# Kernel tuning notes

Hardware: AMD Instinct MI355X
Metric: run time of the kernel (lower is better)

Reference implementation:

```python
import jax, jax.numpy as jnp
import numpy as np

B, N_IN, HID, N_OUT = 1024, 512, 64, 256


def setup_inputs() -> dict:
    key = jax.random.key(0)
    ks = jax.random.split(key, 10)
    s = 0.02
    return {
        "x": jax.random.normal(ks[0], (B, N_IN), dtype=jnp.float32),
        "ln_gamma": jnp.ones((N_IN,), dtype=jnp.float32),
        "ln_beta": jnp.zeros((N_IN,), dtype=jnp.float32),
        "Wq": jax.random.normal(ks[1], (N_IN, HID * N_OUT), dtype=jnp.float32) * s,
        "bq": jnp.zeros((HID * N_OUT,), dtype=jnp.float32),
        "Wk": jax.random.normal(ks[2], (N_IN, HID * N_OUT), dtype=jnp.float32) * s,
        "bk": jnp.zeros((HID * N_OUT,), dtype=jnp.float32),
        "Wv": jax.random.normal(ks[3], (N_IN, HID * N_OUT), dtype=jnp.float32) * s,
        "bv": jnp.zeros((HID * N_OUT,), dtype=jnp.float32),
        "Wo": jax.random.normal(ks[4], (HID, N_OUT), dtype=jnp.float32) * s,
        "bo": jnp.zeros((N_OUT,), dtype=jnp.float32),
    }


def reference(x, ln_gamma, ln_beta, Wq, bq, Wk, bk, Wv, bv, Wo, bo):
    # LayerNorm over last dim (input_shape)
    mu = jnp.mean(x, axis=-1, keepdims=True)
    var = jnp.mean(jnp.square(x - mu), axis=-1, keepdims=True)
    h = (x - mu) / jnp.sqrt(var + 1e-5) * ln_gamma + ln_beta  # (B, 512)

    # QKV projections, then view as (B, N_OUT, HID)
    q = (h @ Wq + bq).reshape(B, N_OUT, HID)
    k = (h @ Wk + bk).reshape(B, N_OUT, HID)
    v = (h @ Wv + bv).reshape(B, N_OUT, HID)

    # Single-head scaled dot-product attention over length N_OUT
    w = jnp.einsum("bqc,bkc->bqk", q, k) * (HID ** -0.5)
    w = jax.nn.softmax(w, axis=2)
    a = jnp.einsum("bqk,bkc->bqc", w, v)  # (B, N_OUT, HID)

    # Output projection, ReLU, negate -> seminegative contact map
    out = jax.nn.relu(a @ Wo + bo)  # (B, N_OUT, N_OUT)
    return -out
```

## Files before the change

kernel.cpp:

```cpp
#include <hip/hip_runtime.h>
#include <hip/hip_fp16.h>

typedef _Float16 h4_t __attribute__((ext_vector_type(4)));
typedef _Float16 h8_t __attribute__((ext_vector_type(8)));
typedef float f4_t __attribute__((ext_vector_type(4)));

#define B_SZ 1024
#define N_IN 512
#define HID 64
#define N_OUT 256
#define QKN (N_OUT * HID)

__global__ __launch_bounds__(256) void k_ln(const float* __restrict__ x,
                                            const float* __restrict__ gamma,
                                            const float* __restrict__ beta,
                                            _Float16* __restrict__ h16) {
    int tid = threadIdx.x;
    int wave = tid >> 6, lane = tid & 63;
    int row = blockIdx.x * 4 + wave;
    const float4* xr = (const float4*)(x + (size_t)row * N_IN);
    float4 a = xr[lane];
    float4 b = xr[lane + 64];
    float s = a.x + a.y + a.z + a.w + b.x + b.y + b.z + b.w;
    float sq = a.x * a.x + a.y * a.y + a.z * a.z + a.w * a.w +
               b.x * b.x + b.y * b.y + b.z * b.z + b.w * b.w;
    for (int off = 1; off < 64; off <<= 1) {
        s += __shfl_xor(s, off);
        sq += __shfl_xor(sq, off);
    }
    float mean = s * (1.0f / N_IN);
    float var = sq * (1.0f / N_IN) - mean * mean;
    float rstd = rsqrtf(var + 1e-5f);
    float4 g0 = ((const float4*)gamma)[lane];
    float4 g1 = ((const float4*)gamma)[lane + 64];
    float4 e0 = ((const float4*)beta)[lane];
    float4 e1 = ((const float4*)beta)[lane + 64];
    h4_t o0 = {(_Float16)((a.x - mean) * rstd * g0.x + e0.x),
               (_Float16)((a.y - mean) * rstd * g0.y + e0.y),
               (_Float16)((a.z - mean) * rstd * g0.z + e0.z),
               (_Float16)((a.w - mean) * rstd * g0.w + e0.w)};
    h4_t o1 = {(_Float16)((b.x - mean) * rstd * g1.x + e1.x),
               (_Float16)((b.y - mean) * rstd * g1.y + e1.y),
               (_Float16)((b.z - mean) * rstd * g1.z + e1.z),
               (_Float16)((b.w - mean) * rstd * g1.w + e1.w)};
    h4_t* hr = (h4_t*)(h16 + (size_t)row * N_IN);
    hr[lane] = o0;
    hr[lane + 64] = o1;
}

__global__ __launch_bounds__(256) void k_wt(const float* __restrict__ Wq,
                                            const float* __restrict__ Wk,
                                            const float* __restrict__ Wv,
                                            _Float16* __restrict__ wt) {
    __shared__ _Float16 t[64][65];
    const float* W = blockIdx.z == 0 ? Wq : (blockIdx.z == 1 ? Wk : Wv);
    _Float16* out = wt + (size_t)blockIdx.z * ((size_t)QKN * N_IN);
    int n0 = blockIdx.x * 64, k0 = blockIdx.y * 64;
    int c = threadIdx.x & 63, rq = threadIdx.x >> 6;
    for (int i = 0; i < 16; i++) {
        int r = i * 4 + rq;
        t[r][c] = (_Float16)W[(size_t)(k0 + r) * QKN + n0 + c];
    }
    __syncthreads();
    for (int i = 0; i < 16; i++) {
        int r = i * 4 + rq;
        out[(size_t)(n0 + r) * N_IN + k0 + c] = t[c][r];
    }
}

__global__ __launch_bounds__(256) void k_qkv(const _Float16* __restrict__ h16,
                                             const _Float16* __restrict__ wt,
                                             const float* __restrict__ bq,
                                             const float* __restrict__ bk,
                                             const float* __restrict__ bv,
                                             _Float16* __restrict__ qkv) {
    __shared__ _Float16 As[2][4096];
    __shared__ _Float16 Bs[2][4096];
    int z = blockIdx.z;
    const _Float16* Wb = wt + (size_t)z * ((size_t)QKN * N_IN);
    const float* bias = z == 0 ? bq : (z == 1 ? bk : bv);
    _Float16* out = qkv + (size_t)z * ((size_t)B_SZ * QKN);
    int m0 = blockIdx.x * 128, n0 = blockIdx.y * 128;
    int tid = threadIdx.x, lane = tid & 63, w = tid >> 6;
    int wm = w & 1, wn = w >> 1;
    int col16 = lane & 15, quad = lane >> 4;

    int idx0 = (w * 2 + 0) * 512 + lane * 8;
    int idx1 = (w * 2 + 1) * 512 + lane * 8;
    int row0 = idx0 >> 5, col0 = idx0 & 31;
    int row1 = idx1 >> 5, col1 = idx1 & 31;
    const _Float16* pa0 = h16 + (size_t)(m0 + row0) * N_IN + col0;
    const _Float16* pa1 = h16 + (size_t)(m0 + row1) * N_IN + col1;
    const _Float16* pb0 = Wb + (size_t)(n0 + row0) * N_IN + col0;
    const _Float16* pb1 = Wb + (size_t)(n0 + row1) * N_IN + col1;

#define STAGE_QKV(buf, kk)                                                          \
    do {                                                                            \
        __builtin_amdgcn_global_load_lds(                                           \
            (const __attribute__((address_space(1))) void*)(pa0 + (kk)),            \
            (__attribute__((address_space(3))) void*)(&As[buf][(w * 2 + 0) * 512]), \
            16, 0, 0);                                                              \
        __builtin_amdgcn_global_load_lds(                                           \
            (const __attribute__((address_space(1))) void*)(pa1 + (kk)),            \
            (__attribute__((address_space(3))) void*)(&As[buf][(w * 2 + 1) * 512]), \
            16, 0, 0);                                                              \
        __builtin_amdgcn_global_load_lds(                                           \
            (const __attribute__((address_space(1))) void*)(pb0 + (kk)),            \
            (__attribute__((address_space(3))) void*)(&Bs[buf][(w * 2 + 0) * 512]), \
            16, 0, 0);                                                              \
        __builtin_amdgcn_global_load_lds(                                           \
            (const __attribute__((address_space(1))) void*)(pb1 + (kk)),            \
            (__attribute__((address_space(3))) void*)(&Bs[buf][(w * 2 + 1) * 512]), \
            16, 0, 0);                                                              \
    } while (0)

#define QKV_COMPUTE(buf)                                                                        \
    do {                                                                                        \
        h8_t af[4], bf[4];                                                                      \
        for (int mt = 0; mt < 4; mt++)                                                          \
            af[mt] = *(const h8_t*)(&As[buf][(wm * 64 + mt * 16 + col16) * 32 + quad * 8]);     \
        for (int nt = 0; nt < 4; nt++)                                                          \
            bf[nt] = *(const h8_t*)(&Bs[buf][(wn * 64 + nt * 16 + col16) * 32 + quad * 8]);     \
        for (int mt = 0; mt < 4; mt++)                                                          \
            for (int nt = 0; nt < 4; nt++)                                                      \
                acc[mt][nt] =                                                                   \
                    __builtin_amdgcn_mfma_f32_16x16x32_f16(bf[nt], af[mt], acc[mt][nt], 0, 0, 0); \
    } while (0)

    f4_t acc[4][4] = {};
    STAGE_QKV(0, 0);
    STAGE_QKV(1, 32);
    for (int t = 0; t < 14; t++) {
        int buf = t & 1;
        asm volatile("s_waitcnt vmcnt(4)" ::: "memory");
        __builtin_amdgcn_s_barrier();
        asm volatile("" ::: "memory");
        QKV_COMPUTE(buf);
        asm volatile("s_waitcnt lgkmcnt(0)" ::: "memory");
        __builtin_amdgcn_s_barrier();
        asm volatile("" ::: "memory");
        STAGE_QKV(buf, (t + 2) * 32);
    }
    asm volatile("s_waitcnt vmcnt(4)" ::: "memory");
    __builtin_amdgcn_s_barrier();
    asm volatile("" ::: "memory");
    QKV_COMPUTE(0);
    asm volatile("s_waitcnt vmcnt(0)" ::: "memory");
    __builtin_amdgcn_s_barrier();
    asm volatile("" ::: "memory");
    QKV_COMPUTE(1);
#undef STAGE_QKV
#undef QKV_COMPUTE

    for (int mt = 0; mt < 4; mt++) {
        int m = m0 + wm * 64 + mt * 16 + col16;
        for (int nt = 0; nt < 4; nt++) {
            int nb = n0 + wn * 64 + nt * 16 + quad * 4;
            f4_t bb = *(const f4_t*)(bias + nb);
            h4_t hv = {(_Float16)(acc[mt][nt][0] + bb[0]),
                       (_Float16)(acc[mt][nt][1] + bb[1]),
                       (_Float16)(acc[mt][nt][2] + bb[2]),
                       (_Float16)(acc[mt][nt][3] + bb[3])};
            *(h4_t*)(out + (size_t)m * QKN + nb) = hv;
        }
    }
}

__global__ __launch_bounds__(512) void k_attn(const _Float16* __restrict__ qkv,
                                              const float* __restrict__ Wo,
                                              const float* __restrict__ bo,
                                              float* __restrict__ out) {
    __shared__ _Float16 lds[32768];
    int b = blockIdx.x;
    int tid = threadIdx.x, lane = tid & 63, w = tid >> 6;
    int col16 = lane & 15, quad = lane >> 4;
    const _Float16* qb = qkv + (size_t)b * QKN;
    const _Float16* kb = qkv + (size_t)(B_SZ + b) * QKN;
    const _Float16* vb = qkv + (size_t)(2 * B_SZ + b) * QKN;

    for (int r = 0; r < 4; r++) {
        int slab = r * 8 + w;
        int c8 = slab >> 2, kblk = slab & 3;
        __builtin_amdgcn_global_load_lds(
            (const __attribute__((address_space(1))) void*)(kb + (size_t)(kblk * 64 + lane) * 64 + c8 * 8),
            (__attribute__((address_space(3))) void*)(lds + slab * 512),
            16, 0, 0);
    }

    int kq_ = lane >> 2, k3 = lane & 3;
    int hb = w & 3, kbase2 = (w >> 2) * 128;
    for (int kc2 = 0; kc2 < 2; kc2++) {
        int key = kbase2 + kc2 * 64 + lane;
        h8_t va = *(const h8_t*)(vb + (size_t)key * 64 + hb * 16);
        h8_t vc = *(const h8_t*)(vb + (size_t)key * 64 + hb * 16 + 8);
        int kq = key >> 2;
        int kx = kq & 7;
        _Float16* vp = lds + 16384 + kq * 256 + k3;
        for (int j = 0; j < 8; j++) vp[(size_t)((hb * 16 + j) ^ kx) * 4] = va[j];
        for (int j = 0; j < 8; j++) vp[(size_t)((hb * 16 + 8 + j) ^ kx) * 4] = vc[j];
    }
    (void)kq_;

    h8_t qf[2][2];
    int qbase = w * 32;
    for (int qt = 0; qt < 2; qt++)
        for (int ki = 0; ki < 2; ki++)
            qf[qt][ki] = *(const h8_t*)(qb + (size_t)(qbase + qt * 16 + col16) * 64 + ki * 32 + quad * 8);

    __syncthreads();

    f4_t o[4][2] = {};
    float lrun[2] = {0.f, 0.f};
    const float sc = 0.125f * 1.44269504f;

    for (int kc = 0; kc < 16; kc++) {
        h8_t kf0 = *(const h8_t*)(lds + (size_t)quad * 2048 + (size_t)(kc * 16 + col16) * 8);
        h8_t kf1 = *(const h8_t*)(lds + (size_t)(4 + quad) * 2048 + (size_t)(kc * 16 + col16) * 8);
        int kqr = kc * 4 + quad, kxr = kqr & 7;
        h4_t vf[4];
        for (int mt = 0; mt < 4; mt++)
            vf[mt] = *(const h4_t*)(lds + 16384 + kqr * 256 +
                                    (size_t)((mt * 16 + col16) ^ kxr) * 4);
        for (int qt = 0; qt < 2; qt++) {
            f4_t s = {};
            s = __builtin_amdgcn_mfma_f32_16x16x32_f16(kf0, qf[qt][0], s, 0, 0, 0);
            s = __builtin_amdgcn_mfma_f32_16x16x32_f16(kf1, qf[qt][1], s, 0, 0, 0);
            float p0 = exp2f(s[0] * sc);
            float p1 = exp2f(s[1] * sc);
            float p2 = exp2f(s[2] * sc);
            float p3 = exp2f(s[3] * sc);
            lrun[qt] += (p0 + p1) + (p2 + p3);
            h4_t pf = {(_Float16)p0, (_Float16)p1, (_Float16)p2, (_Float16)p3};
            for (int mt = 0; mt < 4; mt++)
                o[mt][qt] = __builtin_amdgcn_mfma_f32_16x16x16f16(vf[mt], pf, o[mt][qt], 0, 0, 0);
        }
    }

    for (int qt = 0; qt < 2; qt++) {
        float l = lrun[qt];
        l += __shfl_xor(l, 16);
        l += __shfl_xor(l, 32);
        lrun[qt] = l;
    }

    h4_t af[2][4];
    for (int qt = 0; qt < 2; qt++) {
        float rl = 1.0f / lrun[qt];
        for (int hk = 0; hk < 4; hk++) {
            f4_t t = o[hk][qt];
            af[qt][hk] = (h4_t){(_Float16)(t[0] * rl), (_Float16)(t[1] * rl),
                                (_Float16)(t[2] * rl), (_Float16)(t[3] * rl)};
        }
    }
    __syncthreads();
    {
        int no = tid & 255, pr = tid >> 8;
        for (int it2 = 0; it2 < 8; it2++) {
            int hh0 = it2 * 8 + pr * 4;
            h4_t wv = {(_Float16)Wo[(size_t)(hh0 + 0) * 256 + no],
                       (_Float16)Wo[(size_t)(hh0 + 1) * 256 + no],
                       (_Float16)Wo[(size_t)(hh0 + 2) * 256 + no],
                       (_Float16)Wo[(size_t)(hh0 + 3) * 256 + no]};
            *(h4_t*)(lds + (it2 * 2 + pr) * 1024 + no * 4) = wv;
        }
    }
    __syncthreads();

    float* outb = out + (size_t)b * (N_OUT * N_OUT);
    for (int nc = 0; nc < 4; nc++) {
        for (int nt = 0; nt < 4; nt++) {
            int no = nc * 64 + nt * 16 + col16;
            h4_t wf[4];
            for (int hk = 0; hk < 4; hk++)
                wf[hk] = *(const h4_t*)(lds + (hk * 4 + quad) * 1024 + no * 4);
            f4_t bb = *(const f4_t*)(bo + nc * 64 + nt * 16 + quad * 4);
            for (int qt = 0; qt < 2; qt++) {
                f4_t a = {};
                for (int hk = 0; hk < 4; hk++)
                    a = __builtin_amdgcn_mfma_f32_16x16x16f16(wf[hk], af[qt][hk], a, 0, 0, 0);
                int q = qbase + qt * 16 + col16;
                int nob = nc * 64 + nt * 16 + quad * 4;
                f4_t v;
                for (int r = 0; r < 4; r++) {
                    float t = a[r] + bb[r];
                    v[r] = (t > 0.f) ? -t : 0.f;
                }
                *(f4_t*)(outb + (size_t)q * N_OUT + nob) = v;
            }
        }
    }
}

extern "C" void kernel_launch(void* const* d_in, const int* in_sizes, int n_in,
                              void* d_out, int out_size, void* d_ws, size_t ws_size,
                              hipStream_t stream) {
    const float* x = (const float*)d_in[0];
    const float* gamma = (const float*)d_in[1];
    const float* beta = (const float*)d_in[2];
    const float* Wq = (const float*)d_in[3];
    const float* bq = (const float*)d_in[4];
    const float* Wk = (const float*)d_in[5];
    const float* bk = (const float*)d_in[6];
    const float* Wv = (const float*)d_in[7];
    const float* bv = (const float*)d_in[8];
    const float* Wo = (const float*)d_in[9];
    const float* bo = (const float*)d_in[10];
    float* out = (float*)d_out;

    _Float16* h16 = (_Float16*)d_ws;
    _Float16* wt16 = h16 + (size_t)B_SZ * N_IN;
    _Float16* qkv16 = wt16 + (size_t)3 * QKN * N_IN;

    k_ln<<<dim3(B_SZ / 4), 256, 0, stream>>>(x, gamma, beta, h16);
    k_wt<<<dim3(QKN / 64, N_IN / 64, 3), 256, 0, stream>>>(Wq, Wk, Wv, wt16);
    k_qkv<<<dim3(B_SZ / 128, QKN / 128, 3), 256, 0, stream>>>(h16, wt16, bq, bk, bv, qkv16);
    k_attn<<<dim3(B_SZ), 512, 0, stream>>>(qkv16, Wo, bo, out);
}
```

Baseline: 509.9 us.

## Triple-buffer QKV GEMM and split output projection into separate kernel

The QKV GEMM main loop moves from double to triple buffering in LDS, keeping two stages of loads in flight, and the loop is fully unrolled. The attention kernel no longer stages K in LDS. It reads K fragments straight from global memory and halves its LDS use, which may raise occupancy. The output projection becomes its own kernel, k_proj, which writes normalized attention output through an fp16 workspace and uses a swizzled Wo tile in LDS. The cost is an extra round trip through global memory for the attention output and one more kernel launch.

After: 545.5 us. +7.0%, slower.

```diff
diff --git a/kernel.cpp b/kernel.cpp
--- a/kernel.cpp
+++ b/kernel.cpp
@@ -74,8 +74,8 @@
                                              const float* __restrict__ bk,
                                              const float* __restrict__ bv,
                                              _Float16* __restrict__ qkv) {
-    __shared__ _Float16 As[2][4096];
-    __shared__ _Float16 Bs[2][4096];
+    __shared__ _Float16 As[3][4096];
+    __shared__ _Float16 Bs[3][4096];
     int z = blockIdx.z;
     const _Float16* Wb = wt + (size_t)z * ((size_t)QKN * N_IN);
     const float* bias = z == 0 ? bq : (z == 1 ? bk : bv);
@@ -114,41 +114,41 @@
             16, 0, 0);                                                              \
     } while (0)
 
-#define QKV_COMPUTE(buf)                                                                        \
-    do {                                                                                        \
-        h8_t af[4], bf[4];                                                                      \
-        for (int mt = 0; mt < 4; mt++)                                                          \
-            af[mt] = *(const h8_t*)(&As[buf][(wm * 64 + mt * 16 + col16) * 32 + quad * 8]);     \
-        for (int nt = 0; nt < 4; nt++)                                                          \
-            bf[nt] = *(const h8_t*)(&Bs[buf][(wn * 64 + nt * 16 + col16) * 32 + quad * 8]);     \
-        for (int mt = 0; mt < 4; mt++)                                                          \
-            for (int nt = 0; nt < 4; nt++)                                                      \
-                acc[mt][nt] =                                                                   \
+#define QKV_COMPUTE(buf)                                                                          \
+    do {                                                                                          \
+        h8_t af[4], bf[4];                                                                        \
+        for (int mt = 0; mt < 4; mt++)                                                            \
+            af[mt] = *(const h8_t*)(&As[buf][(wm * 64 + mt * 16 + col16) * 32 + quad * 8]);       \
+        for (int nt = 0; nt < 4; nt++)                                                            \
+            bf[nt] = *(const h8_t*)(&Bs[buf][(wn * 64 + nt * 16 + col16) * 32 + quad * 8]);       \
+        for (int mt = 0; mt < 4; mt++)                                                            \
+            for (int nt = 0; nt < 4; nt++)                                                        \
+                acc[mt][nt] =                                                                     \
                     __builtin_amdgcn_mfma_f32_16x16x32_f16(bf[nt], af[mt], acc[mt][nt], 0, 0, 0); \
     } while (0)
 
     f4_t acc[4][4] = {};
     STAGE_QKV(0, 0);
     STAGE_QKV(1, 32);
-    for (int t = 0; t < 14; t++) {
-        int buf = t & 1;
-        asm volatile("s_waitcnt vmcnt(4)" ::: "memory");
+    STAGE_QKV(2, 64);
+#pragma unroll
+    for (int t = 0; t < 16; t++) {
+        int bi = t % 3;
+        if (t <= 13) {
+            asm volatile("s_waitcnt vmcnt(8)" ::: "memory");
+        } else if (t == 14) {
+            asm volatile("s_waitcnt vmcnt(4)" ::: "memory");
+        } else {
+            asm volatile("s_waitcnt vmcnt(0)" ::: "memory");
+        }
         __builtin_amdgcn_s_barrier();
         asm volatile("" ::: "memory");
-        QKV_COMPUTE(buf);
+        QKV_COMPUTE(bi);
         asm volatile("s_waitcnt lgkmcnt(0)" ::: "memory");
         __builtin_amdgcn_s_barrier();
         asm volatile("" ::: "memory");
-        STAGE_QKV(buf, (t + 2) * 32);
-    }
-    asm volatile("s_waitcnt vmcnt(4)" ::: "memory");
-    __builtin_amdgcn_s_barrier();
-    asm volatile("" ::: "memory");
-    QKV_COMPUTE(0);
-    asm volatile("s_waitcnt vmcnt(0)" ::: "memory");
-    __builtin_amdgcn_s_barrier();
-    asm volatile("" ::: "memory");
-    QKV_COMPUTE(1);
+        if (t + 3 <= 15) STAGE_QKV(bi, (t + 3) * 32);
+    }
 #undef STAGE_QKV
 #undef QKV_COMPUTE
 
@@ -167,10 +167,8 @@
 }
 
 __global__ __launch_bounds__(512) void k_attn(const _Float16* __restrict__ qkv,
-                                              const float* __restrict__ Wo,
-                                              const float* __restrict__ bo,
-                                              float* __restrict__ out) {
-    __shared__ _Float16 lds[32768];
+                                              _Float16* __restrict__ a16) {
+    __shared__ _Float16 lds[16384];
     int b = blockIdx.x;
     int tid = threadIdx.x, lane = tid & 63, w = tid >> 6;
     int col16 = lane & 15, quad = lane >> 4;
@@ -178,16 +176,7 @@
     const _Float16* kb = qkv + (size_t)(B_SZ + b) * QKN;
     const _Float16* vb = qkv + (size_t)(2 * B_SZ + b) * QKN;
 
-    for (int r = 0; r < 4; r++) {
-        int slab = r * 8 + w;
-        int c8 = slab >> 2, kblk = slab & 3;
-        __builtin_amdgcn_global_load_lds(
-            (const __attribute__((address_space(1))) void*)(kb + (size_t)(kblk * 64 + lane) * 64 + c8 * 8),
-            (__attribute__((address_space(3))) void*)(lds + slab * 512),
-            16, 0, 0);
-    }
-
-    int kq_ = lane >> 2, k3 = lane & 3;
+    int k3 = lane & 3;
     int hb = w & 3, kbase2 = (w >> 2) * 128;
     for (int kc2 = 0; kc2 < 2; kc2++) {
         int key = kbase2 + kc2 * 64 + lane;
@@ -195,11 +184,10 @@
         h8_t vc = *(const h8_t*)(vb + (size_t)key * 64 + hb * 16 + 8);
         int kq = key >> 2;
         int kx = kq & 7;
-        _Float16* vp = lds + 16384 + kq * 256 + k3;
+        _Float16* vp = lds + kq * 256 + k3;
         for (int j = 0; j < 8; j++) vp[(size_t)((hb * 16 + j) ^ kx) * 4] = va[j];
         for (int j = 0; j < 8; j++) vp[(size_t)((hb * 16 + 8 + j) ^ kx) * 4] = vc[j];
     }
-    (void)kq_;
 
     h8_t qf[2][2];
     int qbase = w * 32;
@@ -214,13 +202,12 @@
     const float sc = 0.125f * 1.44269504f;
 
     for (int kc = 0; kc < 16; kc++) {
-        h8_t kf0 = *(const h8_t*)(lds + (size_t)quad * 2048 + (size_t)(kc * 16 + col16) * 8);
-        h8_t kf1 = *(const h8_t*)(lds + (size_t)(4 + quad) * 2048 + (size_t)(kc * 16 + col16) * 8);
+        h8_t kf0 = *(const h8_t*)(kb + (size_t)(kc * 16 + col16) * 64 + quad * 8);
+        h8_t kf1 = *(const h8_t*)(kb + (size_t)(kc * 16 + col16) * 64 + 32 + quad * 8);
         int kqr = kc * 4 + quad, kxr = kqr & 7;
         h4_t vf[4];
         for (int mt = 0; mt < 4; mt++)
-            vf[mt] = *(const h4_t*)(lds + 16384 + kqr * 256 +
-                                    (size_t)((mt * 16 + col16) ^ kxr) * 4);
+            vf[mt] = *(const h4_t*)(lds + kqr * 256 + (size_t)((mt * 16 + col16) ^ kxr) * 4);
         for (int qt = 0; qt < 2; qt++) {
             f4_t s = {};
             s = __builtin_amdgcn_mfma_f32_16x16x32_f16(kf0, qf[qt][0], s, 0, 0, 0);
@@ -240,53 +227,70 @@
         float l = lrun[qt];
         l += __shfl_xor(l, 16);
         l += __shfl_xor(l, 32);
-        lrun[qt] = l;
-    }
-
-    h4_t af[2][4];
-    for (int qt = 0; qt < 2; qt++) {
-        float rl = 1.0f / lrun[qt];
-        for (int hk = 0; hk < 4; hk++) {
-            f4_t t = o[hk][qt];
-            af[qt][hk] = (h4_t){(_Float16)(t[0] * rl), (_Float16)(t[1] * rl),
-                                (_Float16)(t[2] * rl), (_Float16)(t[3] * rl)};
+        float rl = 1.0f / l;
+        int q = qbase + qt * 16 + col16;
+        _Float16* ap = a16 + ((size_t)b * N_OUT + q) * HID + quad * 4;
+        for (int mt = 0; mt < 4; mt++) {
+            f4_t t = o[mt][qt];
+            h4_t hv = {(_Float16)(t[0] * rl), (_Float16)(t[1] * rl),
+                       (_Float16)(t[2] * rl), (_Float16)(t[3] * rl)};
+            *(h4_t*)(ap + mt * 16) = hv;
+        }
+    }
+}
+
+__global__ __launch_bounds__(512) void k_proj(const _Float16* __restrict__ a16,
+                                              const float* __restrict__ Wo,
+                                              const float* __restrict__ bo,
+                                              float* __restrict__ out) {
+    __shared__ _Float16 wt[16384];
+    int tid = threadIdx.x, lane = tid & 63, w = tid >> 6;
+    int col16 = lane & 15, quad = lane >> 4;
+    int wm = w & 1, wn = w >> 1;
+    int m0 = blockIdx.x * 128;
+
+    {
+        int n = tid & 255, pr = tid >> 8;
+        for (int it = 0; it < 8; it++) {
+            int h0 = it * 8 + pr * 4;
+            h4_t wv = {(_Float16)Wo[(size_t)(h0 + 0) * 256 + n],
+                       (_Float16)Wo[(size_t)(h0 + 1) * 256 + n],
+                       (_Float16)Wo[(size_t)(h0 + 2) * 256 + n],
+                       (_Float16)Wo[(size_t)(h0 + 3) * 256 + n]};
+            *(h4_t*)(wt + n * 64 + (h0 ^ ((n & 7) << 3))) = wv;
         }
     }
     __syncthreads();
-    {
-        int no = tid & 255, pr = tid >> 8;
-        for (int it2 = 0; it2 < 8; it2++) {
-            int hh0 = it2 * 8 + pr * 4;
-            h4_t wv = {(_Float16)Wo[(size_t)(hh0 + 0) * 256 + no],
-                       (_Float16)Wo[(size_t)(hh0 + 1) * 256 + no],
-                       (_Float16)Wo[(size_t)(hh0 + 2) * 256 + no],
-                       (_Float16)Wo[(size_t)(hh0 + 3) * 256 + no]};
-            *(h4_t*)(lds + (it2 * 2 + pr) * 1024 + no * 4) = wv;
-        }
-    }
-    __syncthreads();
-
-    float* outb = out + (size_t)b * (N_OUT * N_OUT);
-    for (int nc = 0; nc < 4; nc++) {
+
+    h8_t bf[4][2];
+    for (int nt = 0; nt < 4; nt++) {
+        int n = wn * 64 + nt * 16 + col16;
+        for (int ki = 0; ki < 2; ki++)
+            bf[nt][ki] = *(const h8_t*)(wt + n * 64 + ((ki * 32 + quad * 8) ^ ((n & 7) << 3)));
+    }
+    h8_t af[4][2];
+    for (int mt = 0; mt < 4; mt++) {
+        int row = m0 + wm * 64 + mt * 16 + col16;
+        for (int ki = 0; ki < 2; ki++)
+            af[mt][ki] = *(const h8_t*)(a16 + (size_t)row * HID + ki * 32 + quad * 8);
+    }
+    f4_t acc[4][4] = {};
+    for (int mt = 0; mt < 4; mt++)
+        for (int nt = 0; nt < 4; nt++)
+            for (int ki = 0; ki < 2; ki++)
+                acc[mt][nt] = __builtin_amdgcn_mfma_f32_16x16x32_f16(bf[nt][ki], af[mt][ki],
+                                                                     acc[mt][nt], 0, 0, 0);
+    for (int mt = 0; mt < 4; mt++) {
+        size_t row = (size_t)(m0 + wm * 64 + mt * 16 + col16);
         for (int nt = 0; nt < 4; nt++) {
-            int no = nc * 64 + nt * 16 + col16;
-            h4_t wf[4];
-            for (int hk = 0; hk < 4; hk++)
-                wf[hk] = *(const h4_t*)(lds + (hk * 4 + quad) * 1024 + no * 4);
-            f4_t bb = *(const f4_t*)(bo + nc * 64 + nt * 16 + quad * 4);
-            for (int qt = 0; qt < 2; qt++) {
-                f4_t a = {};
-                for (int hk = 0; hk < 4; hk++)
-                    a = __builtin_amdgcn_mfma_f32_16x16x16f16(wf[hk], af[qt][hk], a, 0, 0, 0);
-                int q = qbase + qt * 16 + col16;
-                int nob = nc * 64 + nt * 16 + quad * 4;
-                f4_t v;
-                for (int r = 0; r < 4; r++) {
-                    float t = a[r] + bb[r];
-                    v[r] = (t > 0.f) ? -t : 0.f;
-                }
-                *(f4_t*)(outb + (size_t)q * N_OUT + nob) = v;
+            int nb = wn * 64 + nt * 16 + quad * 4;
+            f4_t bb = *(const f4_t*)(bo + nb);
+            f4_t v;
+            for (int r = 0; r < 4; r++) {
+                float t = acc[mt][nt][r] + bb[r];
+                v[r] = (t > 0.f) ? -t : 0.f;
             }
+            *(f4_t*)(out + row * N_OUT + nb) = v;
         }
     }
 }
@@ -310,9 +314,11 @@
     _Float16* h16 = (_Float16*)d_ws;
     _Float16* wt16 = h16 + (size_t)B_SZ * N_IN;
     _Float16* qkv16 = wt16 + (size_t)3 * QKN * N_IN;
+    _Float16* a16 = qkv16 + (size_t)3 * B_SZ * QKN;
 
     k_ln<<<dim3(B_SZ / 4), 256, 0, stream>>>(x, gamma, beta, h16);
     k_wt<<<dim3(QKN / 64, N_IN / 64, 3), 256, 0, stream>>>(Wq, Wk, Wv, wt16);
     k_qkv<<<dim3(B_SZ / 128, QKN / 128, 3), 256, 0, stream>>>(h16, wt16, bq, bk, bv, qkv16);
-    k_attn<<<dim3(B_SZ), 512, 0, stream>>>(qkv16, Wo, bo, out);
-}
+    k_attn<<<dim3(B_SZ), 512, 0, stream>>>(qkv16, a16);
+    k_proj<<<dim3((B_SZ * N_OUT) / 128), 512, 0, stream>>>(a16, Wo, bo, out);
+}
```

## Enlarge QKV GEMM tile to 256x128 with 512 threads and swap grid order

Applied to the files above, without the earlier changes.

The QKV projection GEMM now uses 256x128 output tiles computed by 8 waves (512 threads) instead of 128x128 tiles with 4 waves. Each B (weight) tile is reused across twice as many rows, which roughly halves weight-matrix reads from global memory. The grid is reordered so that blocks adjacent in x share the same h rows and walk along N, which may improve L2 locality. The pipeline tail is folded into the main loop with adjusted vmcnt waits. In exchange, LDS use per block rises and the number of blocks halves.

Measured after the change: 498.8 us. -2.2%, faster.

```diff
diff --git a/kernel.cpp b/kernel.cpp
--- a/kernel.cpp
+++ b/kernel.cpp
@@ -68,87 +68,77 @@
     }
 }
 
-__global__ __launch_bounds__(256) void k_qkv(const _Float16* __restrict__ h16,
-                                             const _Float16* __restrict__ wt,
-                                             const float* __restrict__ bq,
-                                             const float* __restrict__ bk,
-                                             const float* __restrict__ bv,
-                                             _Float16* __restrict__ qkv) {
-    __shared__ _Float16 As[2][4096];
+__global__ __launch_bounds__(512, 4) void k_qkv(const _Float16* __restrict__ h16,
+                                                const _Float16* __restrict__ wt,
+                                                const float* __restrict__ bq,
+                                                const float* __restrict__ bk,
+                                                const float* __restrict__ bv,
+                                                _Float16* __restrict__ qkv) {
+    __shared__ _Float16 As[2][8192];
     __shared__ _Float16 Bs[2][4096];
     int z = blockIdx.z;
     const _Float16* Wb = wt + (size_t)z * ((size_t)QKN * N_IN);
     const float* bias = z == 0 ? bq : (z == 1 ? bk : bv);
     _Float16* out = qkv + (size_t)z * ((size_t)B_SZ * QKN);
-    int m0 = blockIdx.x * 128, n0 = blockIdx.y * 128;
+    int n0 = blockIdx.x * 128;
+    int m0 = blockIdx.y * 256;
     int tid = threadIdx.x, lane = tid & 63, w = tid >> 6;
-    int wm = w & 1, wn = w >> 1;
+    int wm = w & 3, wn = w >> 2;
     int col16 = lane & 15, quad = lane >> 4;
 
-    int idx0 = (w * 2 + 0) * 512 + lane * 8;
-    int idx1 = (w * 2 + 1) * 512 + lane * 8;
-    int row0 = idx0 >> 5, col0 = idx0 & 31;
-    int row1 = idx1 >> 5, col1 = idx1 & 31;
-    const _Float16* pa0 = h16 + (size_t)(m0 + row0) * N_IN + col0;
-    const _Float16* pa1 = h16 + (size_t)(m0 + row1) * N_IN + col1;
-    const _Float16* pb0 = Wb + (size_t)(n0 + row0) * N_IN + col0;
-    const _Float16* pb1 = Wb + (size_t)(n0 + row1) * N_IN + col1;
-
-#define STAGE_QKV(buf, kk)                                                          \
-    do {                                                                            \
-        __builtin_amdgcn_global_load_lds(                                           \
-            (const __attribute__((address_space(1))) void*)(pa0 + (kk)),            \
-            (__attribute__((address_space(3))) void*)(&As[buf][(w * 2 + 0) * 512]), \
-            16, 0, 0);                                                              \
-        __builtin_amdgcn_global_load_lds(                                           \
-            (const __attribute__((address_space(1))) void*)(pa1 + (kk)),            \
-            (__attribute__((address_space(3))) void*)(&As[buf][(w * 2 + 1) * 512]), \
-            16, 0, 0);                                                              \
-        __builtin_amdgcn_global_load_lds(                                           \
-            (const __attribute__((address_space(1))) void*)(pb0 + (kk)),            \
-            (__attribute__((address_space(3))) void*)(&Bs[buf][(w * 2 + 0) * 512]), \
-            16, 0, 0);                                                              \
-        __builtin_amdgcn_global_load_lds(                                           \
-            (const __attribute__((address_space(1))) void*)(pb1 + (kk)),            \
-            (__attribute__((address_space(3))) void*)(&Bs[buf][(w * 2 + 1) * 512]), \
-            16, 0, 0);                                                              \
+    int arow = tid >> 2;
+    int acol = (tid & 3) * 8;
+    const _Float16* pa0 = h16 + (size_t)(m0 + arow) * N_IN + acol;
+    const _Float16* pa1 = h16 + (size_t)(m0 + 128 + arow) * N_IN + acol;
+    const _Float16* pb0 = Wb + (size_t)(n0 + arow) * N_IN + acol;
+
+#define STAGE_QKV(buf, kk)                                                   \
+    do {                                                                     \
+        __builtin_amdgcn_global_load_lds(                                    \
+            (const __attribute__((address_space(1))) void*)(pa0 + (kk)),     \
+            (__attribute__((address_space(3))) void*)(&As[buf][w * 512]),    \
+            16, 0, 0);                                                       \
+        __builtin_amdgcn_global_load_lds(                                    \
+            (const __attribute__((address_space(1))) void*)(pa1 + (kk)),     \
+            (__attribute__((address_space(3))) void*)(&As[buf][4096 + w * 512]), \
+            16, 0, 0);                                                       \
+        __builtin_amdgcn_global_load_lds(                                    \
+            (const __attribute__((address_space(1))) void*)(pb0 + (kk)),     \
+            (__attribute__((address_space(3))) void*)(&Bs[buf][w * 512]),    \
+            16, 0, 0);                                                       \
     } while (0)
 
-#define QKV_COMPUTE(buf)                                                                        \
-    do {                                                                                        \
-        h8_t af[4], bf[4];                                                                      \
-        for (int mt = 0; mt < 4; mt++)                                                          \
-            af[mt] = *(const h8_t*)(&As[buf][(wm * 64 + mt * 16 + col16) * 32 + quad * 8]);     \
-        for (int nt = 0; nt < 4; nt++)                                                          \
-            bf[nt] = *(const h8_t*)(&Bs[buf][(wn * 64 + nt * 16 + col16) * 32 + quad * 8]);     \
-        for (int mt = 0; mt < 4; mt++)                                                          \
-            for (int nt = 0; nt < 4; nt++)                                                      \
-                acc[mt][nt] =                                                                   \
+#define QKV_COMPUTE(buf)                                                                          \
+    do {                                                                                          \
+        h8_t af[4], bf[4];                                                                        \
+        for (int mt = 0; mt < 4; mt++)                                                            \
+            af[mt] = *(const h8_t*)(&As[buf][(wm * 64 + mt * 16 + col16) * 32 + quad * 8]);       \
+        for (int nt = 0; nt < 4; nt++)                                                            \
+            bf[nt] = *(const h8_t*)(&Bs[buf][(wn * 64 + nt * 16 + col16) * 32 + quad * 8]);       \
+        for (int mt = 0; mt < 4; mt++)                                                            \
+            for (int nt = 0; nt < 4; nt++)                                                        \
+                acc[mt][nt] =                                                                     \
                     __builtin_amdgcn_mfma_f32_16x16x32_f16(bf[nt], af[mt], acc[mt][nt], 0, 0, 0); \
     } while (0)
 
     f4_t acc[4][4] = {};
     STAGE_QKV(0, 0);
     STAGE_QKV(1, 32);
-    for (int t = 0; t < 14; t++) {
+    for (int t = 0; t < 16; t++) {
         int buf = t & 1;
-        asm volatile("s_waitcnt vmcnt(4)" ::: "memory");
+        if (t < 15) {
+            asm volatile("s_waitcnt vmcnt(3)" ::: "memory");
+        } else {
+            asm volatile("s_waitcnt vmcnt(0)" ::: "memory");
+        }
         __builtin_amdgcn_s_barrier();
         asm volatile("" ::: "memory");
         QKV_COMPUTE(buf);
         asm volatile("s_waitcnt lgkmcnt(0)" ::: "memory");
         __builtin_amdgcn_s_barrier();
         asm volatile("" ::: "memory");
-        STAGE_QKV(buf, (t + 2) * 32);
-    }
-    asm volatile("s_waitcnt vmcnt(4)" ::: "memory");
-    __builtin_amdgcn_s_barrier();
-    asm volatile("" ::: "memory");
-    QKV_COMPUTE(0);
-    asm volatile("s_waitcnt vmcnt(0)" ::: "memory");
-    __builtin_amdgcn_s_barrier();
-    asm volatile("" ::: "memory");
-    QKV_COMPUTE(1);
+        if (t + 2 <= 15) STAGE_QKV(buf, (t + 2) * 32);
+    }
 #undef STAGE_QKV
 #undef QKV_COMPUTE
 
@@ -187,7 +177,7 @@
             16, 0, 0);
     }
 
-    int kq_ = lane >> 2, k3 = lane & 3;
+    int k3 = lane & 3;
     int hb = w & 3, kbase2 = (w >> 2) * 128;
     for (int kc2 = 0; kc2 < 2; kc2++) {
         int key = kbase2 + kc2 * 64 + lane;
@@ -199,7 +189,6 @@
         for (int j = 0; j < 8; j++) vp[(size_t)((hb * 16 + j) ^ kx) * 4] = va[j];
         for (int j = 0; j < 8; j++) vp[(size_t)((hb * 16 + 8 + j) ^ kx) * 4] = vc[j];
     }
-    (void)kq_;
 
     h8_t qf[2][2];
     int qbase = w * 32;
@@ -313,6 +302,6 @@
 
     k_ln<<<dim3(B_SZ / 4), 256, 0, stream>>>(x, gamma, beta, h16);
     k_wt<<<dim3(QKN / 64, N_IN / 64, 3), 256, 0, stream>>>(Wq, Wk, Wv, wt16);
-    k_qkv<<<dim3(B_SZ / 128, QKN / 128, 3), 256, 0, stream>>>(h16, wt16, bq, bk, bv, qkv16);
+    k_qkv<<<dim3(QKN / 128, B_SZ / 256, 3), 512, 0, stream>>>(h16, wt16, bq, bk, bv, qkv16);
     k_attn<<<dim3(B_SZ), 512, 0, stream>>>(qkv16, Wo, bo, out);
 }
```
